# Optimization experiments

Measured on AMD Instinct MI355X. Metric: run time of the kernel, lower is better.

The kernel has to match this reference:

```python
import jax, jax.numpy as jnp
import numpy as np

IGNORE = 255


def setup_inputs() -> dict:
    key = jax.random.key(0)
    k1, k2 = jax.random.split(key)
    B, C, H, W = 4, 19, 512, 512
    out = jax.random.normal(k1, (B, C, H, W), dtype=jnp.float32)
    gt = jax.random.randint(k2, (B, H, W), 0, C, dtype=jnp.int64)
    return {"out": out, "gt": gt}


def _lovasz_softmax_flat(probas, labels):
    # probas: [P, C] softmax probabilities, labels: [P] int
    P, C = probas.shape
    valid = labels != IGNORE  # [P]
    # per-class foreground indicator (masked by valid)
    fg = ((labels[:, None] == jnp.arange(C)[None, :]) & valid[:, None]).astype(probas.dtype)  # [P, C]
    errors = jnp.abs(fg - probas)  # [P, C], values in [0, 1]
    # push ignored pixels to the end of the descending sort (error < 0)
    errors = jnp.where(valid[:, None], errors, -1.0)
    order = jnp.argsort(-errors, axis=0)  # [P, C] descending perm per class
    errors_sorted = jnp.take_along_axis(errors, order, axis=0)
    fg_sorted = jnp.take_along_axis(fg, order, axis=0)
    valid_sorted = jnp.take_along_axis(jnp.broadcast_to(valid[:, None], (P, C)), order, axis=0)
    # zero out ignored pixels' (suffix) contribution
    errors_sorted = jnp.where(valid_sorted, errors_sorted, 0.0)
    # lovasz_grad per class (ignored suffix has fg=0 and errors=0, so it is inert)
    gts = jnp.sum(fg_sorted, axis=0)  # [C]
    csum_fg = jnp.cumsum(fg_sorted, axis=0)
    intersection = gts[None, :] - csum_fg
    union = gts[None, :] + jnp.cumsum(1.0 - fg_sorted, axis=0)
    jaccard = 1.0 - intersection / union
    grad = jnp.concatenate([jaccard[:1], jnp.diff(jaccard, axis=0)], axis=0)  # [P, C]
    loss_c = jnp.sum(errors_sorted * grad, axis=0)  # [C]
    # classes='present': average over classes that appear among valid pixels
    present = gts > 0
    n_present = jnp.maximum(jnp.sum(present.astype(probas.dtype)), 1.0)
    return jnp.sum(jnp.where(present, loss_c, 0.0)) / n_present


def reference(out, gt):
    B, C, H, W = out.shape
    probas = jax.nn.softmax(out, axis=1)  # [B, C, H, W]
    probas_flat = jnp.transpose(probas, (0, 2, 3, 1)).reshape(-1, C)  # [P, C]
    labels_flat = gt.reshape(-1)  # [P]
    return _lovasz_softmax_flat(probas_flat, labels_flat)
```

## Files before the change

### kernel.cpp

```cpp
#include <hip/hip_runtime.h>
#include <stdint.h>


#define IGNORE_LBL 255
typedef unsigned long long u64;
constexpr int C_CLS = 19;
constexpr int NB = 256;
constexpr int NBT = C_CLS * NB;
constexpr int HW_C = 512 * 512;
constexpr int HIST_GRID = 512;
constexpr int HIST_NT = 1024;
constexpr int RED_Q = 8;
constexpr float ESCALE = 262144.f;

__device__ __forceinline__ int err_bin(float e) {
    unsigned u = __float_as_uint(e);
    if (u >= 0x3F800000u) return NB - 1;
    if (u < 0x3C000000u) return 0;
    int m = (int)(u >> 23) - 119;
    return (1 << m) - 1 + (int)((u & 0x7FFFFFu) >> (23 - m));
}

__global__ __launch_bounds__(HIST_NT)
void lovasz_hist_kernel(const float* __restrict__ logits,
                        const int* __restrict__ gt,
                        u64* __restrict__ part,
                        int P) {
    __shared__ u64 h[NBT];
    for (int i = threadIdx.x; i < NBT; i += HIST_NT) h[i] = 0ull;
    __syncthreads();

    const int stride = gridDim.x * blockDim.x;
    for (int p = blockIdx.x * blockDim.x + threadIdx.x; p < P; p += stride) {
        int lbl = gt[p];
        if (lbl == IGNORE_LBL) continue;
        int b = p >> 18;
        int hw = p & (HW_C - 1);
        const float* base = logits + (size_t)b * C_CLS * HW_C + hw;

        float v[C_CLS];
        float mx = -3.4e38f;
#pragma unroll
        for (int c = 0; c < C_CLS; ++c) {
            v[c] = base[(size_t)c * HW_C];
            mx = fmaxf(mx, v[c]);
        }
        float s = 0.f;
#pragma unroll
        for (int c = 0; c < C_CLS; ++c) {
            v[c] = __expf(v[c] - mx);
            s += v[c];
        }
        float inv = 1.0f / s;

#pragma unroll
        for (int c = 0; c < C_CLS; ++c) {
            float prob = v[c] * inv;
            bool fg = (c == lbl);
            float e = fg ? (1.0f - prob) : prob;
            e = fmaxf(e, 0.0f);
            unsigned eq = __float2uint_rn(e * ESCALE);
            int bin = c * NB + err_bin(e);
            u64 add = (u64)eq | (1ull << 32) | (fg ? (1ull << 46) : 0ull);
            atomicAdd(&h[bin], add);
        }
    }
    __syncthreads();

    const size_t base_out = (size_t)blockIdx.x * NBT;
    for (int i = threadIdx.x; i < NBT; i += HIST_NT) part[base_out + i] = h[i];
}

__global__ __launch_bounds__(256)
void lovasz_reduce_kernel(const u64* __restrict__ part,
                          u64* __restrict__ red_es,
                          u64* __restrict__ red_cf) {
    const int q = blockIdx.x / C_CLS;
    const int seg = blockIdx.x % C_CLS;
    const int bin = seg * NB + threadIdx.x;
    const int p0 = q * (HIST_GRID / RED_Q);
    u64 es = 0; unsigned cn = 0, fgc = 0;
#pragma unroll 4
    for (int p = p0; p < p0 + HIST_GRID / RED_Q; ++p) {
        u64 x = part[(size_t)p * NBT + bin];
        es += x & 0xFFFFFFFFull;
        cn += (unsigned)((x >> 32) & 0x3FFFu);
        fgc += (unsigned)(x >> 46);
    }
    red_es[(size_t)q * NBT + bin] = es;
    red_cf[(size_t)q * NBT + bin] = (u64)cn | ((u64)fgc << 32);
}

__global__ __launch_bounds__(NB)
void lovasz_scan_kernel(const u64* __restrict__ red_es,
                        const u64* __restrict__ red_cf,
                        float* __restrict__ class_loss,
                        int* __restrict__ class_present) {
    const int c = blockIdx.x;
    const int t = threadIdx.x;
    const int lane = t & 63;
    const int wave = t >> 6;

    __shared__ u64 wtot[4];
    __shared__ u64 sh_total;

    const int db = NB - 1 - t;
    const size_t bo = (size_t)c * NB + db;
    u64 es = 0, nf = 0;
#pragma unroll
    for (int q = 0; q < RED_Q; ++q) {
        es += red_es[(size_t)q * NBT + bo];
        nf += red_cf[(size_t)q * NBT + bo];
    }
    const double mys = (double)es * (1.0 / (double)ESCALE);

    u64 incl = nf;
#pragma unroll
    for (int o = 1; o < 64; o <<= 1) {
        u64 u = __shfl_up(incl, o, 64);
        if (lane >= o) incl += u;
    }
    if (lane == 63) wtot[wave] = incl;
    __syncthreads();
    if (t == 0) {
        u64 run = 0;
#pragma unroll
        for (int w = 0; w < 4; ++w) { u64 x = wtot[w]; wtot[w] = run; run += x; }
        sh_total = run;
    }
    __syncthreads();

    const long long G = (long long)(sh_total >> 32);
    const u64 excl = wtot[wave] + (incl - nf);

    double lsum = 0.0;
    {
        long long n_b = (long long)(nf & 0xffffffffull);
        if (n_b > 0 && G > 0) {
            long long f_b = (long long)(nf >> 32);
            long long k0 = (long long)(excl & 0xffffffffull);
            long long F0 = (long long)(excl >> 32);
            long long I0 = G - F0;
            long long U0 = G + k0 - F0;
            long long F1 = F0 + f_b;
            long long I1 = G - F1;
            long long U1 = G + (k0 + n_b) - F1;
            double dJ = (double)(I0 * U1 - I1 * U0) / ((double)U0 * (double)U1);
            lsum = (mys / (double)n_b) * dJ;
        }
    }

    __shared__ double dred[4];
#pragma unroll
    for (int o = 32; o > 0; o >>= 1) lsum += __shfl_down(lsum, o, 64);
    if (lane == 0) dred[wave] = lsum;
    __syncthreads();
    if (t == 0) {
        double tot = dred[0] + dred[1] + dred[2] + dred[3];
        class_loss[c] = (float)tot;
        class_present[c] = (G > 0) ? 1 : 0;
    }
}

__global__ void lovasz_final_kernel(const float* __restrict__ class_loss,
                                    const int* __restrict__ class_present,
                                    float* __restrict__ out) {
    int t = threadIdx.x;
    float l = 0.f; int pr = 0;
    if (t < C_CLS) { pr = class_present[t]; l = pr ? class_loss[t] : 0.f; }
#pragma unroll
    for (int o = 32; o > 0; o >>= 1) {
        l += __shfl_down(l, o, 64);
        pr += __shfl_down(pr, o, 64);
    }
    if (t == 0) out[0] = l / fmaxf((float)pr, 1.0f);
}

extern "C" void kernel_launch(void* const* d_in, const int* in_sizes, int n_in,
                              void* d_out, int out_size, void* d_ws, size_t ws_size,
                              hipStream_t stream) {
    const float* logits = (const float*)d_in[0];
    const int* gt = (const int*)d_in[1];
    float* out = (float*)d_out;
    const int P = in_sizes[1];

    size_t partBytes = (size_t)HIST_GRID * NBT * sizeof(u64);
    size_t partPad = (partBytes + 255) & ~(size_t)255;
    size_t redBytes = (size_t)RED_Q * NBT * sizeof(u64);
    size_t redPad = (redBytes + 255) & ~(size_t)255;
    u64* part = (u64*)d_ws;
    u64* red_es = (u64*)((char*)d_ws + partPad);
    u64* red_cf = (u64*)((char*)d_ws + partPad + redPad);
    float* class_loss = (float*)((char*)d_ws + partPad + 2 * redPad);
    int* class_present = (int*)((char*)d_ws + partPad + 2 * redPad + 256);

    lovasz_hist_kernel<<<HIST_GRID, HIST_NT, 0, stream>>>(logits, gt, part, P);
    lovasz_reduce_kernel<<<RED_Q * C_CLS, 256, 0, stream>>>(part, red_es, red_cf);
    lovasz_scan_kernel<<<C_CLS, NB, 0, stream>>>(red_es, red_cf, class_loss, class_present);
    lovasz_final_kernel<<<1, 64, 0, stream>>>(class_loss, class_present, out);
}
```

Before: 130.4 us.

## Vectorize histogram loads to two pixels per thread and fuse final reduction into scan

The histogram kernel drops its grid-stride loop. Each thread now handles exactly two adjacent pixels with float2 logit loads and an int2 label load, which relies on P equalling HIST_GRID*HIST_NT*2. The final single-block kernel is removed: scan blocks atomically add their class loss and presence count, and the last-finishing block writes the mean, with the accumulators zeroed in the reduce kernel. This cuts per-iteration loop overhead and one kernel launch, but it hardcodes the problem size and sums class losses in float atomics, whose order is nondeterministic.

Result: no change. 129.9 us (-0.4%).

```diff
diff --git a/kernel.cpp b/kernel.cpp
--- a/kernel.cpp
+++ b/kernel.cpp
@@ -24,45 +24,58 @@
 __global__ __launch_bounds__(HIST_NT)
 void lovasz_hist_kernel(const float* __restrict__ logits,
                         const int* __restrict__ gt,
-                        u64* __restrict__ part,
-                        int P) {
+                        u64* __restrict__ part) {
     __shared__ u64 h[NBT];
     for (int i = threadIdx.x; i < NBT; i += HIST_NT) h[i] = 0ull;
     __syncthreads();
 
-    const int stride = gridDim.x * blockDim.x;
-    for (int p = blockIdx.x * blockDim.x + threadIdx.x; p < P; p += stride) {
-        int lbl = gt[p];
-        if (lbl == IGNORE_LBL) continue;
-        int b = p >> 18;
-        int hw = p & (HW_C - 1);
-        const float* base = logits + (size_t)b * C_CLS * HW_C + hw;
-
-        float v[C_CLS];
-        float mx = -3.4e38f;
-#pragma unroll
-        for (int c = 0; c < C_CLS; ++c) {
-            v[c] = base[(size_t)c * HW_C];
-            mx = fmaxf(mx, v[c]);
-        }
-        float s = 0.f;
-#pragma unroll
-        for (int c = 0; c < C_CLS; ++c) {
-            v[c] = __expf(v[c] - mx);
-            s += v[c];
-        }
-        float inv = 1.0f / s;
-
-#pragma unroll
-        for (int c = 0; c < C_CLS; ++c) {
-            float prob = v[c] * inv;
-            bool fg = (c == lbl);
-            float e = fg ? (1.0f - prob) : prob;
-            e = fmaxf(e, 0.0f);
+    const int gid = blockIdx.x * HIST_NT + threadIdx.x;
+    const int p0 = gid * 2;
+    const int b = p0 >> 18;
+    const int hw = p0 & (HW_C - 1);
+    const float2* base =
+        (const float2*)(logits + (size_t)b * C_CLS * HW_C + hw);
+
+    float2 v[C_CLS];
+    float mx0 = -3.4e38f, mx1 = -3.4e38f;
+#pragma unroll
+    for (int c = 0; c < C_CLS; ++c) {
+        v[c] = base[(size_t)c * (HW_C / 2)];
+        mx0 = fmaxf(mx0, v[c].x);
+        mx1 = fmaxf(mx1, v[c].y);
+    }
+    float s0 = 0.f, s1 = 0.f;
+#pragma unroll
+    for (int c = 0; c < C_CLS; ++c) {
+        v[c].x = __expf(v[c].x - mx0);
+        v[c].y = __expf(v[c].y - mx1);
+        s0 += v[c].x;
+        s1 += v[c].y;
+    }
+    const float inv0 = 1.0f / s0;
+    const float inv1 = 1.0f / s1;
+
+    const int2 lbl2 = *(const int2*)(gt + p0);
+    const bool val0 = (lbl2.x != IGNORE_LBL);
+    const bool val1 = (lbl2.y != IGNORE_LBL);
+
+#pragma unroll
+    for (int c = 0; c < C_CLS; ++c) {
+        if (val0) {
+            float prob = v[c].x * inv0;
+            bool fg = (c == lbl2.x);
+            float e = fmaxf(fg ? (1.0f - prob) : prob, 0.0f);
             unsigned eq = __float2uint_rn(e * ESCALE);
-            int bin = c * NB + err_bin(e);
             u64 add = (u64)eq | (1ull << 32) | (fg ? (1ull << 46) : 0ull);
-            atomicAdd(&h[bin], add);
+            atomicAdd(&h[c * NB + err_bin(e)], add);
+        }
+        if (val1) {
+            float prob = v[c].y * inv1;
+            bool fg = (c == lbl2.y);
+            float e = fmaxf(fg ? (1.0f - prob) : prob, 0.0f);
+            unsigned eq = __float2uint_rn(e * ESCALE);
+            u64 add = (u64)eq | (1ull << 32) | (fg ? (1ull << 46) : 0ull);
+            atomicAdd(&h[c * NB + err_bin(e)], add);
         }
     }
     __syncthreads();
@@ -74,7 +87,9 @@
 __global__ __launch_bounds__(256)
 void lovasz_reduce_kernel(const u64* __restrict__ part,
                           u64* __restrict__ red_es,
-                          u64* __restrict__ red_cf) {
+                          u64* __restrict__ red_cf,
+                          unsigned* __restrict__ acc) {
+    if (blockIdx.x == 0 && threadIdx.x < 4) acc[threadIdx.x] = 0u;
     const int q = blockIdx.x / C_CLS;
     const int seg = blockIdx.x % C_CLS;
     const int bin = seg * NB + threadIdx.x;
@@ -94,8 +109,10 @@
 __global__ __launch_bounds__(NB)
 void lovasz_scan_kernel(const u64* __restrict__ red_es,
                         const u64* __restrict__ red_cf,
-                        float* __restrict__ class_loss,
-                        int* __restrict__ class_present) {
+                        float* __restrict__ loss_acc,
+                        int* __restrict__ pres_acc,
+                        unsigned* __restrict__ done_ctr,
+                        float* __restrict__ out) {
     const int c = blockIdx.x;
     const int t = threadIdx.x;
     const int lane = t & 63;
@@ -157,23 +174,18 @@
     __syncthreads();
     if (t == 0) {
         double tot = dred[0] + dred[1] + dred[2] + dred[3];
-        class_loss[c] = (float)tot;
-        class_present[c] = (G > 0) ? 1 : 0;
-    }
-}
-
-__global__ void lovasz_final_kernel(const float* __restrict__ class_loss,
-                                    const int* __restrict__ class_present,
-                                    float* __restrict__ out) {
-    int t = threadIdx.x;
-    float l = 0.f; int pr = 0;
-    if (t < C_CLS) { pr = class_present[t]; l = pr ? class_loss[t] : 0.f; }
-#pragma unroll
-    for (int o = 32; o > 0; o >>= 1) {
-        l += __shfl_down(l, o, 64);
-        pr += __shfl_down(pr, o, 64);
-    }
-    if (t == 0) out[0] = l / fmaxf((float)pr, 1.0f);
+        if (G > 0) {
+            atomicAdd(loss_acc, (float)tot);
+            atomicAdd(pres_acc, 1);
+        }
+        __threadfence();
+        unsigned d = atomicAdd(done_ctr, 1u);
+        if (d == C_CLS - 1) {
+            float lv = atomicAdd(loss_acc, 0.0f);
+            int pv = atomicAdd(pres_acc, 0);
+            out[0] = lv / fmaxf((float)pv, 1.0f);
+        }
+    }
 }
 
 extern "C" void kernel_launch(void* const* d_in, const int* in_sizes, int n_in,
@@ -182,7 +194,6 @@
     const float* logits = (const float*)d_in[0];
     const int* gt = (const int*)d_in[1];
     float* out = (float*)d_out;
-    const int P = in_sizes[1];
 
     size_t partBytes = (size_t)HIST_GRID * NBT * sizeof(u64);
     size_t partPad = (partBytes + 255) & ~(size_t)255;
@@ -191,11 +202,13 @@
     u64* part = (u64*)d_ws;
     u64* red_es = (u64*)((char*)d_ws + partPad);
     u64* red_cf = (u64*)((char*)d_ws + partPad + redPad);
-    float* class_loss = (float*)((char*)d_ws + partPad + 2 * redPad);
-    int* class_present = (int*)((char*)d_ws + partPad + 2 * redPad + 256);
-
-    lovasz_hist_kernel<<<HIST_GRID, HIST_NT, 0, stream>>>(logits, gt, part, P);
-    lovasz_reduce_kernel<<<RED_Q * C_CLS, 256, 0, stream>>>(part, red_es, red_cf);
-    lovasz_scan_kernel<<<C_CLS, NB, 0, stream>>>(red_es, red_cf, class_loss, class_present);
-    lovasz_final_kernel<<<1, 64, 0, stream>>>(class_loss, class_present, out);
-}
+    unsigned* acc = (unsigned*)((char*)d_ws + partPad + 2 * redPad);
+    float* loss_acc = (float*)&acc[0];
+    int* pres_acc = (int*)&acc[1];
+    unsigned* done_ctr = &acc[2];
+
+    lovasz_hist_kernel<<<HIST_GRID, HIST_NT, 0, stream>>>(logits, gt, part);
+    lovasz_reduce_kernel<<<RED_Q * C_CLS, 256, 0, stream>>>(part, red_es, red_cf, acc);
+    lovasz_scan_kernel<<<C_CLS, NB, 0, stream>>>(red_es, red_cf,
+                                                 loss_acc, pres_acc, done_ctr, out);
+}
```
